# Kernel tuning notes

Measured on AMD Instinct MI355X. Metric: run time of the kernel, lower is better.

The kernel has to match this reference:

```python
import jax, jax.numpy as jnp
import numpy as np

D_MODEL = 1024
N_EXPERTS = 4
TOP_K = 32


def setup_inputs() -> dict:
    key = jax.random.key(0)
    k1, k2, k3, k4 = jax.random.split(key, 4)
    b, t, d = 2, 2048, D_MODEL
    n_lts = 8192
    h = jax.random.normal(k1, (b, t, d), dtype=jnp.float32)
    lts = jax.random.normal(k2, (1, n_lts, d), dtype=jnp.float32)
    # router: nn.Linear(d_model, n_experts)
    lim = 1.0 / np.sqrt(d)
    W_router = jax.random.uniform(k3, (N_EXPERTS, d), minval=-lim, maxval=lim, dtype=jnp.float32)
    b_router = jax.random.uniform(k4, (N_EXPERTS,), minval=-lim, maxval=lim, dtype=jnp.float32)
    return {"h": h, "lts": lts, "W_router": W_router, "b_router": b_router}


def reference(h, lts, W_router, b_router):
    b, t, d = h.shape
    n_lts = lts.shape[1]
    top_k = TOP_K
    n_experts = N_EXPERTS

    # router (eval mode: no noise)
    logits = jnp.einsum('btd,ed->bte', h, W_router) + b_router  # (b,t,E)
    expert_weights = jax.nn.softmax(logits, axis=-1)
    expert_idx = jnp.argmax(expert_weights, axis=-1)            # (b,t) int

    entries_per_expert = n_lts // n_experts
    offsets = jnp.minimum(expert_idx * entries_per_expert, n_lts - top_k)  # (b,t)
    indices = offsets[..., None] + jnp.arange(top_k)            # (b,t,k)
    indices = jnp.minimum(indices, n_lts - 1)

    # gather memory slices: lts broadcast over batch -> (b,t,k,d)
    selected = jnp.take(lts[0], indices, axis=0)

    # small attention of each token over its top_k memory entries
    scores = jnp.einsum('btd,btkd->btk', h, selected) / jnp.sqrt(jnp.asarray(d, h.dtype))
    attn = jax.nn.softmax(scores, axis=-1)
    result = jnp.einsum('btk,btkd->btd', attn, selected)
    return result, expert_weights
```

## Files before the change

### kernel.cpp

```cpp
#include <hip/hip_runtime.h>
#include <hip/hip_fp16.h>
#include <math.h>

constexpr int D    = 1024;
constexpr int NEXP = 4;
constexpr int EPP  = 2048;

typedef _Float16 f16x8 __attribute__((ext_vector_type(8)));
typedef float    f32x4 __attribute__((ext_vector_type(4)));

__device__ __forceinline__ unsigned pk2(float a, float b) {
    return __builtin_bit_cast(unsigned, __builtin_amdgcn_cvt_pkrtz(a, b));
}
__device__ __forceinline__ f16x8 cvt8(const float* p) {
    const float4 u = *reinterpret_cast<const float4*>(p);
    const float4 v = *reinterpret_cast<const float4*>(p + 4);
    const uint4 w = make_uint4(pk2(u.x, u.y), pk2(u.z, u.w), pk2(v.x, v.y), pk2(v.z, v.w));
    return __builtin_bit_cast(f16x8, w);
}

__global__ __launch_bounds__(256) void prep_kernel(
    const float* __restrict__ lts, _Float16* __restrict__ lts16,
    _Float16* __restrict__ ltsT)
{
    const int e = blockIdx.x >> 4, part = (blockIdx.x >> 2) & 3, dc = blockIdx.x & 3;
    const int tid = threadIdx.x;
    __shared__ __align__(16) _Float16 s[8][256];

    const float4* src = reinterpret_cast<const float4*>(lts);
    #pragma unroll
    for (int i = 0; i < 2; ++i) {
        const int f = tid + 256 * i;
        const int r = f >> 6, c4 = f & 63;
        const float4 v = src[(size_t)(e * EPP + part * 8 + r) * 256 + dc * 64 + c4];
        *reinterpret_cast<uint2*>(&s[r][c4 * 4]) = make_uint2(pk2(v.x, v.y), pk2(v.z, v.w));
    }
    __syncthreads();

    {
        const int r = tid >> 5, c = tid & 31;
        *reinterpret_cast<uint4*>(lts16 + (size_t)(e * 32 + part * 8 + r) * D + dc * 256 + c * 8) =
            *reinterpret_cast<const uint4*>(&s[r][c * 8]);
    }
    {
        _Float16 tmp[8];
        #pragma unroll
        for (int k = 0; k < 8; ++k) tmp[k] = s[k][tid];
        *reinterpret_cast<uint4*>(ltsT + ((size_t)e << 15) + (size_t)(dc * 256 + tid) * 32 + part * 8) =
            *reinterpret_cast<const uint4*>(tmp);
    }
}

__global__ __launch_bounds__(256) void qkpv_kernel(
    const float* __restrict__ h, const _Float16* __restrict__ lts16,
    const _Float16* __restrict__ ltsT, const float* __restrict__ Wr,
    const float* __restrict__ br, float* __restrict__ out_res,
    float* __restrict__ out_ew, int ntok, int chunks)
{
    const int e = blockIdx.x / chunks;
    const int chunk = blockIdx.x - e * chunks;
    const int base = chunk * 16;

    const int tid = threadIdx.x, wid = tid >> 6, lane = tid & 63;
    __shared__ int eix[16];
    __shared__ float S_part[4][16][33];
    __shared__ __align__(16) _Float16 P[16][32];

    {
        const float4* h4 = reinterpret_cast<const float4*>(h);
        const float4* w4 = reinterpret_cast<const float4*>(Wr);
        float4 wf[NEXP][4];
        #pragma unroll
        for (int e2 = 0; e2 < NEXP; ++e2)
            #pragma unroll
            for (int i = 0; i < 4; ++i)
                wf[e2][i] = w4[e2 * 256 + lane + 64 * i];
        const float bb0 = br[0], bb1 = br[1], bb2 = br[2], bb3 = br[3];

        #pragma unroll
        for (int t = 0; t < 4; ++t) {
            const int tok = base + wid * 4 + t;
            if (tok < ntok) {
                float acc[NEXP] = {0.f, 0.f, 0.f, 0.f};
                #pragma unroll
                for (int i = 0; i < 4; ++i) {
                    const float4 a = h4[(size_t)tok * 256 + lane + 64 * i];
                    #pragma unroll
                    for (int e2 = 0; e2 < NEXP; ++e2)
                        acc[e2] += a.x * wf[e2][i].x + a.y * wf[e2][i].y
                                 + a.z * wf[e2][i].z + a.w * wf[e2][i].w;
                }
                #pragma unroll
                for (int m = 1; m < 64; m <<= 1)
                    #pragma unroll
                    for (int e2 = 0; e2 < NEXP; ++e2) acc[e2] += __shfl_xor(acc[e2], m);

                const float l0 = acc[0] + bb0, l1 = acc[1] + bb1,
                            l2 = acc[2] + bb2, l3 = acc[3] + bb3;
                const float lm = fmaxf(fmaxf(l0, l1), fmaxf(l2, l3));
                const float e0 = __expf(l0 - lm), e1 = __expf(l1 - lm),
                            e2v = __expf(l2 - lm), e3 = __expf(l3 - lm);
                const float einv = 1.f / (e0 + e1 + e2v + e3);
                int bi = 0; float bv = l0;
                if (l1 > bv) { bv = l1; bi = 1; }
                if (l2 > bv) { bv = l2; bi = 2; }
                if (l3 > bv) { bv = l3; bi = 3; }
                if (bi == e && lane < NEXP) {
                    const float ev = (lane == 0) ? e0 : (lane == 1) ? e1 : (lane == 2) ? e2v : e3;
                    out_ew[(size_t)tok * NEXP + lane] = ev * einv;
                }
                if (lane == 0) eix[wid * 4 + t] = bi;
            } else if (lane == 0) eix[wid * 4 + t] = -1;
        }
    }
    __syncthreads();

    const int rA = lane & 15, g4 = lane >> 4;
    int hr = base + rA; if (hr > ntok - 1) hr = ntok - 1;
    const float*    ap  = h     + (size_t)hr * D + g4 * 8;
    const _Float16* b0p = lts16 + (size_t)(e * 32 + rA) * D + g4 * 8;
    const _Float16* b1p = b0p + 16 * D;

    f32x4 s0 = {0.f, 0.f, 0.f, 0.f}, s1 = {0.f, 0.f, 0.f, 0.f};
    #pragma unroll
    for (int k = 0; k < 8; ++k) {
        const int kc = wid * 8 + k;
        const f16x8 a  = cvt8(ap + kc * 32);
        const f16x8 b0 = *reinterpret_cast<const f16x8*>(b0p + kc * 32);
        const f16x8 b1 = *reinterpret_cast<const f16x8*>(b1p + kc * 32);
        s0 = __builtin_amdgcn_mfma_f32_16x16x32_f16(a, b0, s0, 0, 0, 0);
        s1 = __builtin_amdgcn_mfma_f32_16x16x32_f16(a, b1, s1, 0, 0, 0);
    }
    #pragma unroll
    for (int r = 0; r < 4; ++r) {
        S_part[wid][g4 * 4 + r][rA]      = s0[r];
        S_part[wid][g4 * 4 + r][rA + 16] = s1[r];
    }
    __syncthreads();

    {
        const int tr = tid >> 4, sl = tid & 15;
        const float v0 = S_part[0][tr][sl] + S_part[1][tr][sl]
                       + S_part[2][tr][sl] + S_part[3][tr][sl];
        const float v1 = S_part[0][tr][sl + 16] + S_part[1][tr][sl + 16]
                       + S_part[2][tr][sl + 16] + S_part[3][tr][sl + 16];
        constexpr float inv32 = 1.f / 32.f;
        float mx = fmaxf(v0, v1);
        #pragma unroll
        for (int m = 1; m < 16; m <<= 1) mx = fmaxf(mx, __shfl_xor(mx, m));
        const float p0 = __expf((v0 - mx) * inv32);
        const float p1 = __expf((v1 - mx) * inv32);
        float sm = p0 + p1;
        #pragma unroll
        for (int m = 1; m < 16; m <<= 1) sm += __shfl_xor(sm, m);
        const float is = 1.f / sm;
        P[tr][sl]      = (_Float16)(p0 * is);
        P[tr][sl + 16] = (_Float16)(p1 * is);
    }
    __syncthreads();

    const f16x8 pa = *reinterpret_cast<const f16x8*>(&P[rA][g4 * 8]);
    const _Float16* vtE = ltsT + ((size_t)e << 15);

    #pragma unroll
    for (int i = 0; i < 16; ++i) {
        const int dimc = wid * 256 + i * 16 + rA;
        const f16x8 bk = *reinterpret_cast<const f16x8*>(vtE + (size_t)dimc * 32 + g4 * 8);
        f32x4 o = {0.f, 0.f, 0.f, 0.f};
        o = __builtin_amdgcn_mfma_f32_16x16x32_f16(pa, bk, o, 0, 0, 0);
        #pragma unroll
        for (int r = 0; r < 4; ++r) {
            const int tr2 = g4 * 4 + r;
            if (base + tr2 < ntok && eix[tr2] == e)
                out_res[(size_t)(base + tr2) * D + dimc] = o[r];
        }
    }
}

extern "C" void kernel_launch(void* const* d_in, const int* in_sizes, int n_in,
                              void* d_out, int out_size, void* d_ws, size_t ws_size,
                              hipStream_t stream) {
    const float* h   = (const float*)d_in[0];
    const float* lts = (const float*)d_in[1];
    const float* Wr  = (const float*)d_in[2];
    const float* br  = (const float*)d_in[3];

    const int ntok = in_sizes[0] / D;
    float* out_res = (float*)d_out;
    float* out_ew  = out_res + (size_t)ntok * D;

    _Float16* lts16 = (_Float16*)d_ws;
    _Float16* ltsT  = lts16 + (size_t)128 * D;

    const int chunks = (ntok + 15) / 16;

    prep_kernel<<<64, 256, 0, stream>>>(lts, lts16, ltsT);
    qkpv_kernel<<<NEXP * chunks, 256, 0, stream>>>(h, lts16, ltsT, Wr, br,
                                                   out_res, out_ew, ntok, chunks);
}
```

Baseline: 40.84 us.

## Move router into prep kernel and compact tokens per expert before attention

The router computation moves out of the attention kernel into the prep kernel, which builds per-expert token lists with shared-memory and global atomics. The attention kernel then handles only tiles of tokens routed to its expert and exits early for empty tiles. Before, every expert's blocks recomputed the router and ran the full QK/PV on all tokens, which wasted about 4x the work. The cost is an extra memset launch, atomics, and gathered row reads and writes through the token index.

Result: slower. 47.08 us (+15.3%).

```diff
diff --git a/kernel.cpp b/kernel.cpp
--- a/kernel.cpp
+++ b/kernel.cpp
@@ -5,6 +5,7 @@
 constexpr int D    = 1024;
 constexpr int NEXP = 4;
 constexpr int EPP  = 2048;
+constexpr int CSTR = 16;
 
 typedef _Float16 f16x8 __attribute__((ext_vector_type(8)));
 typedef float    f32x4 __attribute__((ext_vector_type(4)));
@@ -19,105 +20,135 @@
     return __builtin_bit_cast(f16x8, w);
 }
 
-__global__ __launch_bounds__(256) void prep_kernel(
-    const float* __restrict__ lts, _Float16* __restrict__ lts16,
-    _Float16* __restrict__ ltsT)
+__global__ __launch_bounds__(256) void prep_router_kernel(
+    const float* __restrict__ h, const float* __restrict__ lts,
+    const float* __restrict__ Wr, const float* __restrict__ br,
+    float* __restrict__ out_ew, int* __restrict__ gcnt, int* __restrict__ list,
+    _Float16* __restrict__ lts16, _Float16* __restrict__ ltsT, int ntok)
 {
-    const int e = blockIdx.x >> 4, part = (blockIdx.x >> 2) & 3, dc = blockIdx.x & 3;
     const int tid = threadIdx.x;
-    __shared__ __align__(16) _Float16 s[8][256];
-
-    const float4* src = reinterpret_cast<const float4*>(lts);
-    #pragma unroll
-    for (int i = 0; i < 2; ++i) {
-        const int f = tid + 256 * i;
-        const int r = f >> 6, c4 = f & 63;
-        const float4 v = src[(size_t)(e * EPP + part * 8 + r) * 256 + dc * 64 + c4];
-        *reinterpret_cast<uint2*>(&s[r][c4 * 4]) = make_uint2(pk2(v.x, v.y), pk2(v.z, v.w));
-    }
-    __syncthreads();
-
-    {
-        const int r = tid >> 5, c = tid & 31;
-        *reinterpret_cast<uint4*>(lts16 + (size_t)(e * 32 + part * 8 + r) * D + dc * 256 + c * 8) =
-            *reinterpret_cast<const uint4*>(&s[r][c * 8]);
-    }
-    {
-        _Float16 tmp[8];
-        #pragma unroll
-        for (int k = 0; k < 8; ++k) tmp[k] = s[k][tid];
-        *reinterpret_cast<uint4*>(ltsT + ((size_t)e << 15) + (size_t)(dc * 256 + tid) * 32 + part * 8) =
-            *reinterpret_cast<const uint4*>(tmp);
-    }
+
+    if (blockIdx.x < 64) {
+        const int e = blockIdx.x >> 4, part = (blockIdx.x >> 2) & 3, dc = blockIdx.x & 3;
+        __shared__ __align__(16) _Float16 s[8][256];
+
+        const float4* src = reinterpret_cast<const float4*>(lts);
+        #pragma unroll
+        for (int i = 0; i < 2; ++i) {
+            const int f = tid + 256 * i;
+            const int r = f >> 6, c4 = f & 63;
+            const float4 v = src[(size_t)(e * EPP + part * 8 + r) * 256 + dc * 64 + c4];
+            *reinterpret_cast<uint2*>(&s[r][c4 * 4]) = make_uint2(pk2(v.x, v.y), pk2(v.z, v.w));
+        }
+        __syncthreads();
+
+        {
+            const int r = tid >> 5, c = tid & 31;
+            *reinterpret_cast<uint4*>(lts16 + (size_t)(e * 32 + part * 8 + r) * D + dc * 256 + c * 8) =
+                *reinterpret_cast<const uint4*>(&s[r][c * 8]);
+        }
+        {
+            _Float16 tmp[8];
+            #pragma unroll
+            for (int k = 0; k < 8; ++k) tmp[k] = s[k][tid];
+            *reinterpret_cast<uint4*>(ltsT + ((size_t)e << 15) + (size_t)(dc * 256 + tid) * 32 + part * 8) =
+                *reinterpret_cast<const uint4*>(tmp);
+        }
+        return;
+    }
+
+    const int wid = tid >> 6, lane = tid & 63;
+    const int blk = blockIdx.x - 64;
+
+    __shared__ int lds_cnt[NEXP];
+    __shared__ int lds_base[NEXP];
+    if (tid < NEXP) lds_cnt[tid] = 0;
+    __syncthreads();
+
+    const float4* h4 = reinterpret_cast<const float4*>(h);
+    const float4* w4 = reinterpret_cast<const float4*>(Wr);
+    float4 wf[NEXP][4];
+    #pragma unroll
+    for (int e2 = 0; e2 < NEXP; ++e2)
+        #pragma unroll
+        for (int i = 0; i < 4; ++i)
+            wf[e2][i] = w4[e2 * 256 + lane + 64 * i];
+    const float bb0 = br[0], bb1 = br[1], bb2 = br[2], bb3 = br[3];
+
+    int mybi[4], myrank[4], mytok[4];
+    #pragma unroll
+    for (int t = 0; t < 4; ++t) {
+        const int tok = blk * 16 + wid * 4 + t;
+        mytok[t] = -1;
+        if (tok < ntok) {
+            float acc[NEXP] = {0.f, 0.f, 0.f, 0.f};
+            #pragma unroll
+            for (int i = 0; i < 4; ++i) {
+                const float4 a = h4[(size_t)tok * 256 + lane + 64 * i];
+                #pragma unroll
+                for (int e2 = 0; e2 < NEXP; ++e2)
+                    acc[e2] += a.x * wf[e2][i].x + a.y * wf[e2][i].y
+                             + a.z * wf[e2][i].z + a.w * wf[e2][i].w;
+            }
+            #pragma unroll
+            for (int m = 1; m < 64; m <<= 1)
+                #pragma unroll
+                for (int e2 = 0; e2 < NEXP; ++e2) acc[e2] += __shfl_xor(acc[e2], m);
+
+            const float l0 = acc[0] + bb0, l1 = acc[1] + bb1,
+                        l2 = acc[2] + bb2, l3 = acc[3] + bb3;
+            const float lm = fmaxf(fmaxf(l0, l1), fmaxf(l2, l3));
+            const float e0 = __expf(l0 - lm), e1 = __expf(l1 - lm),
+                        e2v = __expf(l2 - lm), e3 = __expf(l3 - lm);
+            const float einv = 1.f / (e0 + e1 + e2v + e3);
+            if (lane < NEXP) {
+                const float ev = (lane == 0) ? e0 : (lane == 1) ? e1 : (lane == 2) ? e2v : e3;
+                out_ew[(size_t)tok * NEXP + lane] = ev * einv;
+            }
+            int bi = 0; float bv = l0;
+            if (l1 > bv) { bv = l1; bi = 1; }
+            if (l2 > bv) { bv = l2; bi = 2; }
+            if (l3 > bv) { bv = l3; bi = 3; }
+            if (lane == 0) {
+                mytok[t] = tok; mybi[t] = bi;
+                myrank[t] = atomicAdd(&lds_cnt[bi], 1);
+            }
+        }
+    }
+    __syncthreads();
+    if (tid < NEXP) lds_base[tid] = atomicAdd(&gcnt[tid * CSTR], lds_cnt[tid]);
+    __syncthreads();
+    #pragma unroll
+    for (int t = 0; t < 4; ++t)
+        if (lane == 0 && mytok[t] >= 0)
+            list[(size_t)mybi[t] * ntok + lds_base[mybi[t]] + myrank[t]] = mytok[t];
 }
 
 __global__ __launch_bounds__(256) void qkpv_kernel(
     const float* __restrict__ h, const _Float16* __restrict__ lts16,
-    const _Float16* __restrict__ ltsT, const float* __restrict__ Wr,
-    const float* __restrict__ br, float* __restrict__ out_res,
-    float* __restrict__ out_ew, int ntok, int chunks)
+    const _Float16* __restrict__ ltsT, const int* __restrict__ gcnt,
+    const int* __restrict__ list, float* __restrict__ out_res,
+    int ntok, int tiles_pe)
 {
-    const int e = blockIdx.x / chunks;
-    const int chunk = blockIdx.x - e * chunks;
-    const int base = chunk * 16;
+    const int e    = blockIdx.x / tiles_pe;
+    const int tile = blockIdx.x - e * tiles_pe;
+    const int n_e  = gcnt[e * CSTR];
+    const int base = tile * 16;
+    if (base >= n_e) return;
 
     const int tid = threadIdx.x, wid = tid >> 6, lane = tid & 63;
-    __shared__ int eix[16];
+    __shared__ int toks[16];
     __shared__ float S_part[4][16][33];
     __shared__ __align__(16) _Float16 P[16][32];
 
-    {
-        const float4* h4 = reinterpret_cast<const float4*>(h);
-        const float4* w4 = reinterpret_cast<const float4*>(Wr);
-        float4 wf[NEXP][4];
-        #pragma unroll
-        for (int e2 = 0; e2 < NEXP; ++e2)
-            #pragma unroll
-            for (int i = 0; i < 4; ++i)
-                wf[e2][i] = w4[e2 * 256 + lane + 64 * i];
-        const float bb0 = br[0], bb1 = br[1], bb2 = br[2], bb3 = br[3];
-
-        #pragma unroll
-        for (int t = 0; t < 4; ++t) {
-            const int tok = base + wid * 4 + t;
-            if (tok < ntok) {
-                float acc[NEXP] = {0.f, 0.f, 0.f, 0.f};
-                #pragma unroll
-                for (int i = 0; i < 4; ++i) {
-                    const float4 a = h4[(size_t)tok * 256 + lane + 64 * i];
-                    #pragma unroll
-                    for (int e2 = 0; e2 < NEXP; ++e2)
-                        acc[e2] += a.x * wf[e2][i].x + a.y * wf[e2][i].y
-                                 + a.z * wf[e2][i].z + a.w * wf[e2][i].w;
-                }
-                #pragma unroll
-                for (int m = 1; m < 64; m <<= 1)
-                    #pragma unroll
-                    for (int e2 = 0; e2 < NEXP; ++e2) acc[e2] += __shfl_xor(acc[e2], m);
-
-                const float l0 = acc[0] + bb0, l1 = acc[1] + bb1,
-                            l2 = acc[2] + bb2, l3 = acc[3] + bb3;
-                const float lm = fmaxf(fmaxf(l0, l1), fmaxf(l2, l3));
-                const float e0 = __expf(l0 - lm), e1 = __expf(l1 - lm),
-                            e2v = __expf(l2 - lm), e3 = __expf(l3 - lm);
-                const float einv = 1.f / (e0 + e1 + e2v + e3);
-                int bi = 0; float bv = l0;
-                if (l1 > bv) { bv = l1; bi = 1; }
-                if (l2 > bv) { bv = l2; bi = 2; }
-                if (l3 > bv) { bv = l3; bi = 3; }
-                if (bi == e && lane < NEXP) {
-                    const float ev = (lane == 0) ? e0 : (lane == 1) ? e1 : (lane == 2) ? e2v : e3;
-                    out_ew[(size_t)tok * NEXP + lane] = ev * einv;
-                }
-                if (lane == 0) eix[wid * 4 + t] = bi;
-            } else if (lane == 0) eix[wid * 4 + t] = -1;
-        }
+    if (tid < 16) {
+        const int idx = base + tid;
+        toks[tid] = list[(size_t)e * ntok + (idx < n_e ? idx : n_e - 1)];
     }
     __syncthreads();
 
     const int rA = lane & 15, g4 = lane >> 4;
-    int hr = base + rA; if (hr > ntok - 1) hr = ntok - 1;
-    const float*    ap  = h     + (size_t)hr * D + g4 * 8;
+    const float*    ap  = h     + (size_t)toks[rA] * D + g4 * 8;
     const _Float16* b0p = lts16 + (size_t)(e * 32 + rA) * D + g4 * 8;
     const _Float16* b1p = b0p + 16 * D;
 
@@ -171,8 +202,8 @@
         #pragma unroll
         for (int r = 0; r < 4; ++r) {
             const int tr2 = g4 * 4 + r;
-            if (base + tr2 < ntok && eix[tr2] == e)
-                out_res[(size_t)(base + tr2) * D + dimc] = o[r];
+            if (base + tr2 < n_e)
+                out_res[(size_t)toks[tr2] * D + dimc] = o[r];
         }
     }
 }
@@ -191,10 +222,16 @@
 
     _Float16* lts16 = (_Float16*)d_ws;
     _Float16* ltsT  = lts16 + (size_t)128 * D;
-
-    const int chunks = (ntok + 15) / 16;
-
-    prep_kernel<<<64, 256, 0, stream>>>(lts, lts16, ltsT);
-    qkpv_kernel<<<NEXP * chunks, 256, 0, stream>>>(h, lts16, ltsT, Wr, br,
-                                                   out_res, out_ew, ntok, chunks);
-}
+    int* gcnt = (int*)(ltsT + (size_t)NEXP * D * 32);
+    int* list = gcnt + NEXP * CSTR;
+
+    (void)hipMemsetAsync(gcnt, 0, NEXP * CSTR * sizeof(int), stream);
+
+    const int rblocks = (ntok + 15) / 16;
+    prep_router_kernel<<<64 + rblocks, 256, 0, stream>>>(h, lts, Wr, br, out_ew,
+                                                         gcnt, list, lts16, ltsT, ntok);
+
+    const int tiles_pe = (ntok + 15) / 16;
+    qkpv_kernel<<<NEXP * tiles_pe, 256, 0, stream>>>(h, lts16, ltsT, gcnt, list,
+                                                     out_res, ntok, tiles_pe);
+}
```
